# Kernel optimization log

Hardware: AMD Instinct MI355X
Metric: run time of the kernel (lower is better)

## Reference

```python
import jax, jax.numpy as jnp
import numpy as np

N_EL, N_NB, DIM = 8192, 24, 256
CUTOFF = 5.0
F0, F1 = 32, 16
N_ENV = 8
N_FEAT = 4  # [dist, dx, dy, dz]


def setup_inputs() -> dict:
    key = jax.random.key(0)
    ks = jax.random.split(key, 24)
    d = {}
    d['elec'] = jax.random.normal(ks[0], (N_EL, DIM), jnp.float32)
    d['msg'] = jax.random.normal(ks[1], (N_EL, DIM), jnp.float32)
    # positions inside a box of half the cutoff so pairs are within range
    d['r'] = jax.random.uniform(ks[2], (N_EL, 3), jnp.float32) * (0.5 * CUTOFF)
    d['r_nb'] = jax.random.uniform(ks[3], (N_EL, N_NB, 3), jnp.float32) * (0.5 * CUTOFF)
    d['s'] = jax.random.randint(ks[4], (N_EL,), 0, 2, jnp.int32)
    d['s_nb'] = jax.random.randint(ks[5], (N_EL, N_NB), 0, 2, jnp.int32)
    d['hinit_nb'] = jax.random.normal(ks[6], (N_EL, N_NB, DIM), jnp.float32)
    # parameters
    def lecun(k, shape):
        fan_in = shape[0]
        return jax.random.normal(k, shape, jnp.float32) / np.float32(np.sqrt(fan_in))
    d['W_in'] = lecun(ks[7], (DIM, DIM)); d['b_in'] = jnp.zeros((DIM,), jnp.float32)
    d['ee_scales'] = jax.random.uniform(ks[8], (N_ENV,), jnp.float32, 0.5, CUTOFF)
    d['ee_kernel'] = lecun(ks[9], (N_FEAT, F0))
    d['ee_bias'] = 2.0 * jax.random.normal(ks[10], (F0,), jnp.float32)
    d['Wf'] = lecun(ks[11], (F0 + N_ENV, F1)); d['bf'] = jnp.zeros((F1,), jnp.float32)
    d['Wsame'] = lecun(ks[12], (F1, DIM))
    d['Wdiff'] = lecun(ks[13], (F1, DIM))
    d['W1'] = lecun(ks[14], (DIM, DIM)); d['b1'] = jnp.zeros((DIM,), jnp.float32)
    d['W2'] = lecun(ks[15], (DIM, DIM)); d['b2'] = jnp.zeros((DIM,), jnp.float32)
    d['W3'] = lecun(ks[16], (DIM, DIM)); d['b3'] = jnp.zeros((DIM,), jnp.float32)
    d['scale'] = jnp.float32(1.0)  # FixedScalingFactor (identity at init)
    return d


def _forward(elec, msg, r, r_nb, s, s_nb, hinit_nb,
             W_in, b_in, ee_scales, ee_kernel, ee_bias, Wf, bf,
             Wsame, Wdiff, W1, b1, W2, b2, W3, b3, scale):
    silu = jax.nn.silu
    elec1 = silu(elec @ W_in + b_in)                       # [N, D]
    # get_diff_features: [dist, dx, dy, dz]
    diff = r_nb - r[:, None, :]                             # [N, K, 3]
    dist = jnp.sqrt(jnp.sum(diff * diff, -1) + 1e-12)       # [N, K]
    feats = jnp.concatenate([dist[..., None], diff], -1)    # [N, K, 4]
    spin_mask = s[:, None] == s_nb                          # [N, K]
    # PairwiseFilter: MLP on diff-features + radial envelopes, smooth cutoff
    env = jnp.exp(-jnp.square(dist[..., None] / ee_scales)) # [N, K, E]
    h = silu(feats @ ee_kernel + ee_bias)                   # [N, K, F0]
    h = jnp.concatenate([h, env], -1)                       # [N, K, F0+E]
    x = dist / CUTOFF
    cut = jnp.where(dist < CUTOFF, jnp.square(1.0 - x) * (1.0 + 2.0 * x), 0.0)
    beta = (h @ Wf + bf) * cut[..., None]                   # [N, K, F1]
    gamma = jnp.where(spin_mask[..., None], beta @ Wsame, beta @ Wdiff)  # [N, K, D]
    hinit_msg = jnp.einsum('nid,nid->nd', silu(elec1[:, None] + hinit_nb), gamma)
    out = silu(elec1 @ W1 + b1 + hinit_msg)
    out = silu(out @ W2 + b2 + msg)
    out = silu(out @ W3 + b3)
    return (out + elec1) * scale


def reference(elec, msg, r, r_nb, s, s_nb, hinit_nb,
              W_in, b_in, ee_scales, ee_kernel, ee_bias, Wf, bf,
              Wsame, Wdiff, W1, b1, W2, b2, W3, b3, scale):
    return _forward(elec, msg, r, r_nb, s, s_nb, hinit_nb,
                    W_in, b_in, ee_scales, ee_kernel, ee_bias, Wf, bf,
                    Wsame, Wdiff, W1, b1, W2, b2, W3, b3, scale)
```

## Files before the change

kernel.cpp:

```cpp
#include <hip/hip_runtime.h>

#define DIM 256
#define PDIM 260
#define PD2  264
#define NNB 24
#define NEL 8192
#define ROWS 16
#define NT 512
#define CUTOFF 5.0f
#define E1_OFF 524288
#define SWP 264

typedef unsigned int u32;
typedef unsigned short u16;
typedef __attribute__((ext_vector_type(8))) short bf16x8;
typedef __attribute__((ext_vector_type(4))) float f32x4;

__device__ __forceinline__ u16 f2b(float f){
  union{float f;u32 i;}v; v.f=f;
  u32 r = v.i + 0x7fffu + ((v.i>>16)&1u);
  return (u16)(r>>16);
}
__device__ __forceinline__ float b2f(u16 u){
  union{u32 i;float f;}v; v.i = ((u32)u)<<16; return v.f;
}
__device__ __forceinline__ float fast_silu(float x){
  float e = __builtin_amdgcn_exp2f(-1.44269504088896340f * x);
  return x * __builtin_amdgcn_rcpf(1.0f + e);
}

__global__ __launch_bounds__(256)
void wprep(const float* __restrict__ W0, const float* __restrict__ W1,
           const float* __restrict__ W2, const float* __restrict__ W3,
           const float* __restrict__ Wsame, const float* __restrict__ Wdiff,
           u16* __restrict__ ws){
  if (blockIdx.x < 1024){
    const int mat = blockIdx.x >> 8;
    const int n   = blockIdx.x & 255;
    const int k   = threadIdx.x;
    const float* W = (mat==0)?W0:(mat==1)?W1:(mat==2)?W2:W3;
    ws[(mat<<16) + (n<<8) + k] = f2b(W[(k<<8) + n]);
  } else {
    const int n = threadIdx.x;
    u16* dst = ws + 4*65536 + n*32;
    #pragma unroll
    for (int kk = 0; kk < 16; kk++){
      dst[kk]    = f2b(Wsame[kk*DIM + n]);
      dst[16+kk] = f2b(Wdiff[kk*DIM + n]);
    }
  }
}

template<int MODE, int ABF16>
__device__ __forceinline__ void gemm_mfma(
    const void* A, u16* sE1b, float* sR1,
    const u16* __restrict__ Wt, const float* __restrict__ bias,
    const float* __restrict__ extraGbl, float* __restrict__ outGbl,
    float scl, int n0, int t)
{
  const int lane = t & 63;
  const int ln   = lane & 15;
  const int quad = lane >> 4;
  const int nt0  = (t >> 6) << 1;
  f32x4 acc0 = {0.f,0.f,0.f,0.f};
  f32x4 acc1 = {0.f,0.f,0.f,0.f};
  const u16* bp0 = Wt + (nt0*16 + ln)*DIM;
  const u16* bp1 = bp0 + 16*DIM;
  #pragma unroll
  for (int ks = 0; ks < 8; ks++){
    const int k0 = ks*32 + quad*8;
    bf16x8 af;
    if (ABF16){
      af = *(const bf16x8*)((const u16*)A + ln*PD2 + k0);
    } else {
      const float* arow = (const float*)A + ln*PDIM;
      float4 a01 = *(const float4*)(arow + k0);
      float4 a23 = *(const float4*)(arow + k0 + 4);
      af[0]=(short)f2b(a01.x); af[1]=(short)f2b(a01.y);
      af[2]=(short)f2b(a01.z); af[3]=(short)f2b(a01.w);
      af[4]=(short)f2b(a23.x); af[5]=(short)f2b(a23.y);
      af[6]=(short)f2b(a23.z); af[7]=(short)f2b(a23.w);
    }
    bf16x8 b0 = *(const bf16x8*)(bp0 + k0);
    bf16x8 b1 = *(const bf16x8*)(bp1 + k0);
    acc0 = __builtin_amdgcn_mfma_f32_16x16x32_bf16(af, b0, acc0, 0, 0, 0);
    acc1 = __builtin_amdgcn_mfma_f32_16x16x32_bf16(af, b1, acc1, 0, 0, 0);
  }
  if (MODE == 2) __syncthreads();
  #pragma unroll
  for (int r = 0; r < 4; r++){
    const int m = quad*4 + r;
    #pragma unroll
    for (int tt = 0; tt < 2; tt++){
      const int n = (nt0+tt)*16 + ln;
      float v = (tt ? acc1[r] : acc0[r]) + bias[n];
      if (MODE == 2) v += extraGbl[(size_t)(n0+m)*DIM + n];
      v = fast_silu(v);
      if (MODE == 3) outGbl[(size_t)(n0+m)*DIM + n] = (v + b2f(sE1b[m*PD2 + n])) * scl;
      else           sR1[m*PDIM + n] = v;
    }
  }
}

__global__ __launch_bounds__(NT, 8)
void k1_gemm1(const float* __restrict__ elec, const float* __restrict__ bin,
              const u16* __restrict__ Wt, u16* __restrict__ elec1g)
{
  const int t  = threadIdx.x;
  const int n0 = blockIdx.x * ROWS;
  const int lane = t & 63;
  const int ln   = lane & 15;
  const int quad = lane >> 4;
  const int nt0  = (t >> 6) << 1;
  f32x4 acc0 = {0.f,0.f,0.f,0.f};
  f32x4 acc1 = {0.f,0.f,0.f,0.f};
  const u16* bp0 = Wt + (nt0*16 + ln)*DIM;
  const u16* bp1 = bp0 + 16*DIM;
  const float* arow = elec + (size_t)(n0 + ln)*DIM;
  #pragma unroll
  for (int ks = 0; ks < 8; ks++){
    const int k0 = ks*32 + quad*8;
    float4 a01 = *(const float4*)(arow + k0);
    float4 a23 = *(const float4*)(arow + k0 + 4);
    bf16x8 af;
    af[0]=(short)f2b(a01.x); af[1]=(short)f2b(a01.y);
    af[2]=(short)f2b(a01.z); af[3]=(short)f2b(a01.w);
    af[4]=(short)f2b(a23.x); af[5]=(short)f2b(a23.y);
    af[6]=(short)f2b(a23.z); af[7]=(short)f2b(a23.w);
    bf16x8 b0 = *(const bf16x8*)(bp0 + k0);
    bf16x8 b1 = *(const bf16x8*)(bp1 + k0);
    acc0 = __builtin_amdgcn_mfma_f32_16x16x32_bf16(af, b0, acc0, 0, 0, 0);
    acc1 = __builtin_amdgcn_mfma_f32_16x16x32_bf16(af, b1, acc1, 0, 0, 0);
  }
  #pragma unroll
  for (int r = 0; r < 4; r++){
    const int m = quad*4 + r;
    #pragma unroll
    for (int tt = 0; tt < 2; tt++){
      const int n = (nt0+tt)*16 + ln;
      float v = fast_silu((tt ? acc1[r] : acc0[r]) + bin[n]);
      elec1g[(size_t)(n0+m)*DIM + n] = f2b(v);
    }
  }
}

__global__ __launch_bounds__(256, 4)
void k2_msg(const float* __restrict__ rpos, const float* __restrict__ rnb,
            const int* __restrict__ s, const int* __restrict__ snb,
            const float* __restrict__ hinit,
            const float* __restrict__ eesc, const float* __restrict__ eek,
            const float* __restrict__ eeb,  const float* __restrict__ Wf,
            const float* __restrict__ bfb,
            const float* __restrict__ Wsame, const float* __restrict__ Wdiff,
            const u16* __restrict__ elec1g, float* __restrict__ hmsg)
{
  __shared__ u16   sWb[32*SWP];
  __shared__ float sPar[824];
  __shared__ float sBeta[NNB*16];
  __shared__ float sRed[4][260];
  __shared__ u32   sMask0;
  const int t    = threadIdx.x;
  const int n    = blockIdx.x;
  const int w    = t >> 6;
  const int lane = t & 63;
  const int c0   = lane << 2;

  ushort4 e1u = *(const ushort4*)(elec1g + (size_t)n*DIM + c0);
  const float* hp = hinit + ((size_t)n*NNB + w*6)*DIM + c0;
  float4 h0 = *(const float4*)(hp + 0*DIM);
  float4 h1 = *(const float4*)(hp + 1*DIM);
  float4 h2 = *(const float4*)(hp + 2*DIM);
  float4 h3 = *(const float4*)(hp + 3*DIM);
  float4 h4 = *(const float4*)(hp + 4*DIM);
  float4 h5 = *(const float4*)(hp + 5*DIM);
  __builtin_amdgcn_sched_barrier(0);

  if (t == 0) sMask0 = 0u;
  #pragma unroll
  for (int it = 0; it < 8; it++){
    const int i = t + it*256;
    const int r  = i >> 6;
    const int c4 = (i & 63) << 2;
    const float* Wsrc = (r < 16) ? (Wsame + r*DIM + c4) : (Wdiff + (r-16)*DIM + c4);
    float4 v = *(const float4*)Wsrc;
    ushort4 b;
    b.x=f2b(v.x); b.y=f2b(v.y); b.z=f2b(v.z); b.w=f2b(v.w);
    *(ushort4*)&sWb[r*SWP + c4] = b;
  }
  for (int i = t; i < 824; i += 256){
    float v;
    if (i < 640)      v = Wf[i];
    else if (i < 768) v = eek[i-640];
    else if (i < 800) v = eeb[i-768];
    else if (i < 816) v = bfb[i-800];
    else              v = eesc[i-816];
    sPar[i] = v;
  }
  __syncthreads();

  if (t < 4*NNB) {
    const int pr = t >> 2;
    const int j4 = t & 3;
    const float* rp  = rpos + n*3;
    const float* rnp = rnb + (n*NNB + pr)*3;
    float dx = rnp[0] - rp[0];
    float dy = rnp[1] - rp[1];
    float dz = rnp[2] - rp[2];
    float dist = sqrtf(dx*dx + dy*dy + dz*dz + 1e-12f);
    float feats[4] = {dist, dx, dy, dz};
    float h[32];
    #pragma unroll
    for (int f4 = 0; f4 < 8; f4++){
      float4 a4 = *(const float4*)&sPar[768 + 4*f4];
      float av[4] = {a4.x, a4.y, a4.z, a4.w};
      #pragma unroll
      for (int i = 0; i < 4; i++){
        float4 kv = *(const float4*)&sPar[640 + i*32 + 4*f4];
        av[0]+=feats[i]*kv.x; av[1]+=feats[i]*kv.y; av[2]+=feats[i]*kv.z; av[3]+=feats[i]*kv.w;
      }
      h[4*f4+0]=fast_silu(av[0]); h[4*f4+1]=fast_silu(av[1]);
      h[4*f4+2]=fast_silu(av[2]); h[4*f4+3]=fast_silu(av[3]);
    }
    float env[8];
    #pragma unroll
    for (int e = 0; e < 8; e++){
      float q = dist * __builtin_amdgcn_rcpf(sPar[816 + e]);
      env[e] = __builtin_amdgcn_exp2f(-1.44269504088896340f * q * q);
    }
    float xx = dist * (1.0f/CUTOFF);
    float cut = (dist < CUTOFF) ? (1.0f-xx)*(1.0f-xx)*(1.0f+2.0f*xx) : 0.0f;
    float4 a4 = *(const float4*)&sPar[800 + 4*j4];
    float av[4] = {a4.x, a4.y, a4.z, a4.w};
    #pragma unroll
    for (int f = 0; f < 40; f++){
      float val = (f < 32) ? h[f] : env[f-32];
      float4 wv = *(const float4*)&sPar[f*16 + 4*j4];
      av[0]+=val*wv.x; av[1]+=val*wv.y; av[2]+=val*wv.z; av[3]+=val*wv.w;
    }
    *(float4*)&sBeta[pr*16 + j4*4] =
        make_float4(av[0]*cut, av[1]*cut, av[2]*cut, av[3]*cut);
    if (j4 == 0 && s[n] == snb[n*NNB + pr]) atomicOr(&sMask0, 1u << pr);
  }
  __syncthreads();

  const u32 mb = sMask0;
  float g[6][4];
  #pragma unroll
  for (int i = 0; i < 6; i++){ g[i][0]=0.f; g[i][1]=0.f; g[i][2]=0.f; g[i][3]=0.f; }
  for (int j = 0; j < 16; j++){
    ushort4 su = *(const ushort4*)&sWb[j*SWP + c0];
    ushort4 du = *(const ushort4*)&sWb[(j+16)*SWP + c0];
    float ws0=b2f(su.x), ws1=b2f(su.y), ws2=b2f(su.z), ws3=b2f(su.w);
    float wd0=b2f(du.x), wd1=b2f(du.y), wd2=b2f(du.z), wd3=b2f(du.w);
    #pragma unroll
    for (int i = 0; i < 6; i++){
      const int k = w*6 + i;
      const float b = sBeta[k*16 + j];
      const bool m = ((mb >> k) & 1u) != 0u;
      g[i][0] += b * (m ? ws0 : wd0);
      g[i][1] += b * (m ? ws1 : wd1);
      g[i][2] += b * (m ? ws2 : wd2);
      g[i][3] += b * (m ? ws3 : wd3);
    }
  }

  float e0=b2f(e1u.x), e1=b2f(e1u.y), e2=b2f(e1u.z), e3=b2f(e1u.w);
  float hm0=0.f, hm1=0.f, hm2=0.f, hm3=0.f;
#define CONSUME(i, hv) \
  hm0 += fast_silu(e0 + hv.x) * g[i][0]; \
  hm1 += fast_silu(e1 + hv.y) * g[i][1]; \
  hm2 += fast_silu(e2 + hv.z) * g[i][2]; \
  hm3 += fast_silu(e3 + hv.w) * g[i][3];
  CONSUME(0, h0) CONSUME(1, h1) CONSUME(2, h2)
  CONSUME(3, h3) CONSUME(4, h4) CONSUME(5, h5)
#undef CONSUME

  *(float4*)&sRed[w][c0] = make_float4(hm0, hm1, hm2, hm3);
  __syncthreads();
  {
    float r = sRed[0][t] + sRed[1][t] + sRed[2][t] + sRed[3][t];
    hmsg[(size_t)n*DIM + t] = r;
  }
}

__global__ __launch_bounds__(NT, 8)
void k3_gemms(const float* __restrict__ msg, const u16* __restrict__ elec1g,
              const float* __restrict__ b1, const float* __restrict__ b2,
              const float* __restrict__ b3, const float* __restrict__ scalep,
              const u16* __restrict__ Wt, float* __restrict__ out)
{
  __shared__ float sR1[ROWS*PDIM];
  __shared__ u16   sE1b[ROWS*PD2];
  const int t  = threadIdx.x;
  const int n0 = blockIdx.x * ROWS;

  {
    const u32* e1u = (const u32*)elec1g;
    #pragma unroll
    for (int h = 0; h < 8; h++){
      const int i   = t + h*NT;
      const int row = i >> 7;
      const int c2  = i & 127;
      *(u32*)&sE1b[row*PD2 + 2*c2] = e1u[(size_t)(n0+row)*128 + c2];
    }
  }
  __syncthreads();

  const float scl = scalep[0];
  gemm_mfma<2,1>(sE1b, sE1b, sR1, Wt + (1<<16), b1, out, nullptr, 0.f, n0, t);
  __syncthreads();
  gemm_mfma<2,0>(sR1, sE1b, sR1, Wt + (2<<16), b2, msg, nullptr, 0.f, n0, t);
  __syncthreads();
  gemm_mfma<3,0>(sR1, sE1b, sR1, Wt + (3<<16), b3, nullptr, out, scl, n0, t);
}

extern "C" void kernel_launch(void* const* d_in, const int* in_sizes, int n_in,
                              void* d_out, int out_size, void* d_ws, size_t ws_size,
                              hipStream_t stream) {
  (void)in_sizes; (void)n_in; (void)ws_size; (void)out_size;
  const float* elec  = (const float*)d_in[0];
  const float* msg   = (const float*)d_in[1];
  const float* rpos  = (const float*)d_in[2];
  const float* rnb   = (const float*)d_in[3];
  const int*   s     = (const int*)d_in[4];
  const int*   snb   = (const int*)d_in[5];
  const float* hinit = (const float*)d_in[6];
  const float* Win   = (const float*)d_in[7];
  const float* bin   = (const float*)d_in[8];
  const float* eesc  = (const float*)d_in[9];
  const float* eek   = (const float*)d_in[10];
  const float* eeb   = (const float*)d_in[11];
  const float* Wf    = (const float*)d_in[12];
  const float* bfb   = (const float*)d_in[13];
  const float* Wsame = (const float*)d_in[14];
  const float* Wdiff = (const float*)d_in[15];
  const float* W1    = (const float*)d_in[16];
  const float* b1    = (const float*)d_in[17];
  const float* W2    = (const float*)d_in[18];
  const float* b2    = (const float*)d_in[19];
  const float* W3    = (const float*)d_in[20];
  const float* b3    = (const float*)d_in[21];
  const float* scl   = (const float*)d_in[22];
  float* outp        = (float*)d_out;
  u16*   wt          = (u16*)d_ws;
  u16*   elec1g      = wt + E1_OFF;

  wprep<<<dim3(1025), dim3(256), 0, stream>>>(Win, W1, W2, W3, Wsame, Wdiff, wt);
  k1_gemm1<<<dim3(NEL/ROWS), dim3(NT), 0, stream>>>(elec, bin, wt, elec1g);
  k2_msg<<<dim3(NEL), dim3(256), 0, stream>>>(
      rpos, rnb, s, snb, hinit, eesc, eek, eeb, Wf, bfb,
      Wsame, Wdiff, elec1g, outp);
  k3_gemms<<<dim3(NEL/ROWS), dim3(NT), 0, stream>>>(
      msg, elec1g, b1, b2, b3, scl, wt, outp);
}
```

Measured before the change: 434.8 us.

## Compute gamma with bf16 MFMA using prepacked Wsame/Wdiff weights

Replaces the per-block conversion of Wsame/Wdiff into shared memory with direct loads of a prepacked bf16 concatenated weight (from the wprep workspace). Gamma for the 24 neighbours is computed with 16x16x32 bf16 MFMAs, with the same/diff spin selection done by masking the beta operand, and written to shared memory. This removes per-block weight conversion and the scalar FMA loop. It adds one extra barrier and relies on wprep having written the concatenated layout at offset 4*65536.

```diff
diff --git a/kernel.cpp b/kernel.cpp
--- a/kernel.cpp
+++ b/kernel.cpp
@@ -9,7 +9,7 @@
 #define NT 512
 #define CUTOFF 5.0f
 #define E1_OFF 524288
-#define SWP 264
+#define SGP 260
 
 typedef unsigned int u32;
 typedef unsigned short u16;
@@ -151,19 +151,24 @@
             const float* __restrict__ eesc, const float* __restrict__ eek,
             const float* __restrict__ eeb,  const float* __restrict__ Wf,
             const float* __restrict__ bfb,
-            const float* __restrict__ Wsame, const float* __restrict__ Wdiff,
+            const u16* __restrict__ Wt,
             const u16* __restrict__ elec1g, float* __restrict__ hmsg)
 {
-  __shared__ u16   sWb[32*SWP];
+  __shared__ float sG[NNB*SGP];
   __shared__ float sPar[824];
-  __shared__ float sBeta[NNB*16];
+  __shared__ u16   sBetaB[32*16];
   __shared__ float sRed[4][260];
   __shared__ u32   sMask0;
   const int t    = threadIdx.x;
   const int n    = blockIdx.x;
   const int w    = t >> 6;
   const int lane = t & 63;
+  const int ln   = lane & 15;
+  const int quad = lane >> 4;
+  const int C0   = w << 6;
   const int c0   = lane << 2;
+
+  const u16* Wcat = Wt + 4*65536;
 
   ushort4 e1u = *(const ushort4*)(elec1g + (size_t)n*DIM + c0);
   const float* hp = hinit + ((size_t)n*NNB + w*6)*DIM + c0;
@@ -173,20 +178,14 @@
   float4 h3 = *(const float4*)(hp + 3*DIM);
   float4 h4 = *(const float4*)(hp + 4*DIM);
   float4 h5 = *(const float4*)(hp + 5*DIM);
+  bf16x8 wv0 = *(const bf16x8*)(Wcat + (C0 + 0*16 + ln)*32 + quad*8);
+  bf16x8 wv1 = *(const bf16x8*)(Wcat + (C0 + 1*16 + ln)*32 + quad*8);
+  bf16x8 wv2 = *(const bf16x8*)(Wcat + (C0 + 2*16 + ln)*32 + quad*8);
+  bf16x8 wv3 = *(const bf16x8*)(Wcat + (C0 + 3*16 + ln)*32 + quad*8);
   __builtin_amdgcn_sched_barrier(0);
 
   if (t == 0) sMask0 = 0u;
-  #pragma unroll
-  for (int it = 0; it < 8; it++){
-    const int i = t + it*256;
-    const int r  = i >> 6;
-    const int c4 = (i & 63) << 2;
-    const float* Wsrc = (r < 16) ? (Wsame + r*DIM + c4) : (Wdiff + (r-16)*DIM + c4);
-    float4 v = *(const float4*)Wsrc;
-    ushort4 b;
-    b.x=f2b(v.x); b.y=f2b(v.y); b.z=f2b(v.z); b.w=f2b(v.w);
-    *(ushort4*)&sWb[r*SWP + c4] = b;
-  }
+  if (t < 128) sBetaB[24*16 + t] = 0;
   for (int i = t; i < 824; i += 256){
     float v;
     if (i < 640)      v = Wf[i];
@@ -237,40 +236,56 @@
       float4 wv = *(const float4*)&sPar[f*16 + 4*j4];
       av[0]+=val*wv.x; av[1]+=val*wv.y; av[2]+=val*wv.z; av[3]+=val*wv.w;
     }
-    *(float4*)&sBeta[pr*16 + j4*4] =
-        make_float4(av[0]*cut, av[1]*cut, av[2]*cut, av[3]*cut);
+    ushort4 bv;
+    bv.x = f2b(av[0]*cut); bv.y = f2b(av[1]*cut);
+    bv.z = f2b(av[2]*cut); bv.w = f2b(av[3]*cut);
+    *(ushort4*)&sBetaB[pr*16 + j4*4] = bv;
     if (j4 == 0 && s[n] == snb[n*NNB + pr]) atomicOr(&sMask0, 1u << pr);
   }
   __syncthreads();
 
-  const u32 mb = sMask0;
-  float g[6][4];
-  #pragma unroll
-  for (int i = 0; i < 6; i++){ g[i][0]=0.f; g[i][1]=0.f; g[i][2]=0.f; g[i][3]=0.f; }
-  for (int j = 0; j < 16; j++){
-    ushort4 su = *(const ushort4*)&sWb[j*SWP + c0];
-    ushort4 du = *(const ushort4*)&sWb[(j+16)*SWP + c0];
-    float ws0=b2f(su.x), ws1=b2f(su.y), ws2=b2f(su.z), ws3=b2f(su.w);
-    float wd0=b2f(du.x), wd1=b2f(du.y), wd2=b2f(du.z), wd3=b2f(du.w);
-    #pragma unroll
-    for (int i = 0; i < 6; i++){
-      const int k = w*6 + i;
-      const float b = sBeta[k*16 + j];
-      const bool m = ((mb >> k) & 1u) != 0u;
-      g[i][0] += b * (m ? ws0 : wd0);
-      g[i][1] += b * (m ? ws1 : wd1);
-      g[i][2] += b * (m ? ws2 : wd2);
-      g[i][3] += b * (m ? ws3 : wd3);
-    }
-  }
+  {
+    const u32 mb = sMask0;
+    bf16x8 r0v = *(const bf16x8*)&sBetaB[ln*16 + (quad&1)*8];
+    bf16x8 r1v = *(const bf16x8*)&sBetaB[(16+ln)*16 + (quad&1)*8];
+    const u16 km0 = (u16)((((u32)(quad>>1) ^ ((mb>>ln)&1u)) != 0u) ? 0xFFFFu : 0u);
+    const u16 km1 = (u16)((((u32)(quad>>1) ^ ((mb>>(16+ln))&1u)) != 0u) ? 0xFFFFu : 0u);
+    bf16x8 bf0, bf1;
+    #pragma unroll
+    for (int j = 0; j < 8; j++){
+      bf0[j] = (short)((u16)r0v[j] & km0);
+      bf1[j] = (short)((u16)r1v[j] & km1);
+    }
+    f32x4 z = {0.f,0.f,0.f,0.f};
+    f32x4 d;
+    const int colw = quad*4;
+    d = __builtin_amdgcn_mfma_f32_16x16x32_bf16(wv0, bf0, z, 0, 0, 0);
+    *(f32x4*)&sG[ln*SGP + C0 + 0*16 + colw] = d;
+    d = __builtin_amdgcn_mfma_f32_16x16x32_bf16(wv0, bf1, z, 0, 0, 0);
+    if (ln < 8) *(f32x4*)&sG[(16+ln)*SGP + C0 + 0*16 + colw] = d;
+    d = __builtin_amdgcn_mfma_f32_16x16x32_bf16(wv1, bf0, z, 0, 0, 0);
+    *(f32x4*)&sG[ln*SGP + C0 + 1*16 + colw] = d;
+    d = __builtin_amdgcn_mfma_f32_16x16x32_bf16(wv1, bf1, z, 0, 0, 0);
+    if (ln < 8) *(f32x4*)&sG[(16+ln)*SGP + C0 + 1*16 + colw] = d;
+    d = __builtin_amdgcn_mfma_f32_16x16x32_bf16(wv2, bf0, z, 0, 0, 0);
+    *(f32x4*)&sG[ln*SGP + C0 + 2*16 + colw] = d;
+    d = __builtin_amdgcn_mfma_f32_16x16x32_bf16(wv2, bf1, z, 0, 0, 0);
+    if (ln < 8) *(f32x4*)&sG[(16+ln)*SGP + C0 + 2*16 + colw] = d;
+    d = __builtin_amdgcn_mfma_f32_16x16x32_bf16(wv3, bf0, z, 0, 0, 0);
+    *(f32x4*)&sG[ln*SGP + C0 + 3*16 + colw] = d;
+    d = __builtin_amdgcn_mfma_f32_16x16x32_bf16(wv3, bf1, z, 0, 0, 0);
+    if (ln < 8) *(f32x4*)&sG[(16+ln)*SGP + C0 + 3*16 + colw] = d;
+  }
+  __syncthreads();
 
   float e0=b2f(e1u.x), e1=b2f(e1u.y), e2=b2f(e1u.z), e3=b2f(e1u.w);
   float hm0=0.f, hm1=0.f, hm2=0.f, hm3=0.f;
-#define CONSUME(i, hv) \
-  hm0 += fast_silu(e0 + hv.x) * g[i][0]; \
-  hm1 += fast_silu(e1 + hv.y) * g[i][1]; \
-  hm2 += fast_silu(e2 + hv.z) * g[i][2]; \
-  hm3 += fast_silu(e3 + hv.w) * g[i][3];
+#define CONSUME(i, hv) { \
+  float4 g = *(const float4*)&sG[(w*6 + (i))*SGP + c0]; \
+  hm0 += fast_silu(e0 + hv.x) * g.x; \
+  hm1 += fast_silu(e1 + hv.y) * g.y; \
+  hm2 += fast_silu(e2 + hv.z) * g.z; \
+  hm3 += fast_silu(e3 + hv.w) * g.w; }
   CONSUME(0, h0) CONSUME(1, h1) CONSUME(2, h2)
   CONSUME(3, h3) CONSUME(4, h4) CONSUME(5, h5)
 #undef CONSUME
@@ -349,7 +364,7 @@
   k1_gemm1<<<dim3(NEL/ROWS), dim3(NT), 0, stream>>>(elec, bin, wt, elec1g);
   k2_msg<<<dim3(NEL), dim3(256), 0, stream>>>(
       rpos, rnb, s, snb, hinit, eesc, eek, eeb, Wf, bfb,
-      Wsame, Wdiff, elec1g, outp);
+      wt, elec1g, outp);
   k3_gemms<<<dim3(NEL/ROWS), dim3(NT), 0, stream>>>(
       msg, elec1g, b1, b2, b3, scl, wt, outp);
 }
```

After: 416.5 us. 1.04x faster.
